# Performance work log

Hardware: AMD Instinct MI355X
Metric: run time of the kernel (lower is better)

Reference implementation:

```python
import jax, jax.numpy as jnp
import numpy as np

N, B, LMAX, DIM, IMG_DIM, LY, H = 32768, 16, 2560, 512, 768, 256, 8


def _layernorm(x, g, b, eps=1e-5):
    mu = jnp.mean(x, axis=-1, keepdims=True)
    var = jnp.mean(jnp.square(x - mu), axis=-1, keepdims=True)
    return (x - mu) * jax.lax.rsqrt(var + eps) * g + b


def setup_inputs() -> dict:
    key = jax.random.key(0)
    ks = jax.random.split(key, 16)
    s = DIM ** -0.5
    # ragged per-batch counts summing to N, all <= LMAX
    counts = np.full(B, N // B, dtype=np.int64)
    counts[: B // 2] += 200
    counts[B // 2:] -= 200
    batch_ids = jnp.asarray(np.repeat(np.arange(B), counts), dtype=jnp.int32)
    return {
        "F": jax.random.normal(ks[0], (N, DIM), jnp.float32),
        "y": jax.random.normal(ks[1], (B, LY, IMG_DIM), jnp.float32),
        "ln_g": jnp.ones((DIM,), jnp.float32),
        "ln_b": jnp.zeros((DIM,), jnp.float32),
        "Wq": jax.random.normal(ks[2], (DIM, DIM), jnp.float32) * s,
        "Wk": jax.random.normal(ks[3], (DIM, DIM), jnp.float32) * s,
        "Wv": jax.random.normal(ks[4], (DIM, DIM), jnp.float32) * s,
        "bq": jnp.zeros((DIM,), jnp.float32),
        "bk": jnp.zeros((DIM,), jnp.float32),
        "bv": jnp.zeros((DIM,), jnp.float32),
        "Wo": jax.random.normal(ks[5], (DIM, DIM), jnp.float32) * s,
        "bo": jnp.zeros((DIM,), jnp.float32),
        "W1": jax.random.normal(ks[6], (DIM, IMG_DIM), jnp.float32) * (IMG_DIM ** -0.5),
        "b1": jnp.zeros((DIM,), jnp.float32),
        "W2": jax.random.normal(ks[7], (DIM, DIM), jnp.float32) * s,
        "b2": jnp.zeros((DIM,), jnp.float32),
        "batch_ids": batch_ids,
        "Lmax": LMAX,
    }


def reference(F, y, ln_g, ln_b, Wq, Wk, Wv, bq, bk, bv, Wo, bo, W1, b1, W2, b2, batch_ids, Lmax):
    Bb, Ly, _ = y.shape
    n, dim = F.shape
    dh = dim // H
    # sparse -> dense: per-token slot index within its batch (batch_ids sorted)
    offsets = jnp.searchsorted(batch_ids, jnp.arange(Bb, dtype=batch_ids.dtype))
    pos = jnp.arange(n, dtype=jnp.int32) - offsets[batch_ids].astype(jnp.int32)
    xd = jnp.zeros((Bb, Lmax, dim), F.dtype).at[batch_ids, pos].set(F)  # [B,Lmax,D]
    # NOTE: self.norm is re-bound in subclass => same LayerNorm used twice
    xd = _layernorm(xd, ln_g, ln_b)
    # MLP fuse of image features: Linear -> GELU(exact) -> Linear
    ym = jax.nn.gelu(y @ W1.T + b1, approximate=False) @ W2.T + b2  # [B,Ly,D]
    # MHA cross-attention (no key_padding_mask: mask arg defaults to None)
    q = (xd @ Wq.T + bq).reshape(Bb, Lmax, H, dh)
    k = (ym @ Wk.T + bk).reshape(Bb, Ly, H, dh)
    v = (ym @ Wv.T + bv).reshape(Bb, Ly, H, dh)
    scores = jnp.einsum("bqhd,bkhd->bhqk", q, k) * (dh ** -0.5)
    attn = jax.nn.softmax(scores, axis=-1)
    o = jnp.einsum("bhqk,bkhd->bqhd", attn, v).reshape(Bb, Lmax, dim)
    o = o @ Wo.T + bo
    out_dense = _layernorm(xd + o, ln_g, ln_b)
    # dense -> sparse gather (equivalent to x_dense[x_mask])
    return out_dense[batch_ids, pos]
```

## Files before the change

kernel.cpp:

```cpp
#include <hip/hip_runtime.h>
#include <stdint.h>

#define NTOK 32768
#define BD   512
#define NB   16
#define LYK  256
#define IMGD 768

typedef __attribute__((ext_vector_type(4))) float f32x4;
typedef __attribute__((ext_vector_type(8))) short s16x8;
typedef __attribute__((ext_vector_type(4))) unsigned short u16x4;
typedef unsigned short u16;

__device__ __forceinline__ float bf2f(u16 u) {
  union { uint32_t i; float f; } v; v.i = ((uint32_t)u) << 16; return v.f;
}
__device__ __forceinline__ u16 f2bf(float f) {
  union { float f; uint32_t i; } v; v.f = f;
  uint32_t r = v.i + 0x7fffu + ((v.i >> 16) & 1u);
  return (u16)(r >> 16);
}
__device__ __forceinline__ void gl_lds16(const u16* g, u16* l) {
  __builtin_amdgcn_global_load_lds(
      (const __attribute__((address_space(1))) uint32_t*)g,
      (__attribute__((address_space(3))) uint32_t*)l, 16, 0, 0);
}
__device__ __forceinline__ f32x4 mfma16(s16x8 a, s16x8 b, f32x4 c) {
  return __builtin_amdgcn_mfma_f32_16x16x32_bf16(a, b, c, 0, 0, 0);
}

__global__ __launch_bounds__(256) void cvt_all(
    const float* __restrict__ wq, const float* __restrict__ wk,
    const float* __restrict__ wv, const float* __restrict__ wo,
    const float* __restrict__ w2, const float* __restrict__ w1,
    const float* __restrict__ y,
    u16* __restrict__ dq, u16* __restrict__ dkv, u16* __restrict__ dwo,
    u16* __restrict__ dw2, u16* __restrict__ dw1, u16* __restrict__ dy) {
  int bid = blockIdx.x;
  const float* s; u16* d; int base;
  if      (bid < 128)  { s = wq; d = dq;            base = 0;   }
  else if (bid < 256)  { s = wk; d = dkv;           base = 128; }
  else if (bid < 384)  { s = wv; d = dkv + 262144;  base = 256; }
  else if (bid < 512)  { s = wo; d = dwo;           base = 384; }
  else if (bid < 640)  { s = w2; d = dw2;           base = 512; }
  else if (bid < 832)  { s = w1; d = dw1;           base = 640; }
  else                 { s = y;  d = dy;            base = 832; }
  int i = ((bid - base) * 256 + threadIdx.x) * 8;
  f32x4 a = *(const f32x4*)(s + i);
  f32x4 b = *(const f32x4*)(s + i + 4);
  s16x8 o;
#pragma unroll
  for (int j = 0; j < 4; ++j) { o[j] = (short)f2bf(a[j]); o[4 + j] = (short)f2bf(b[j]); }
  *(s16x8*)(d + i) = o;
}

__global__ void calc_off(const int* __restrict__ bids, int* __restrict__ off) {
  int b = threadIdx.x;
  if (b > NB) return;
  int lo = 0, hi = NTOK;
  while (lo < hi) { int mid = (lo + hi) >> 1; if (bids[mid] < b) lo = mid + 1; else hi = mid; }
  off[b] = lo;
}

__global__ __launch_bounds__(256) void ln_f32_bf16(const float* __restrict__ X,
                                                   const float* __restrict__ g,
                                                   const float* __restrict__ be,
                                                   u16* __restrict__ out) {
  const int lane = threadIdx.x & 63;
  const size_t row = (size_t)blockIdx.x * 4 + (threadIdx.x >> 6);
  const float* x = X + row * BD + lane * 8;
  f32x4 a = *(const f32x4*)x;
  f32x4 b = *(const f32x4*)(x + 4);
  float v[8] = {a[0], a[1], a[2], a[3], b[0], b[1], b[2], b[3]};
  float s = 0.f, s2 = 0.f;
#pragma unroll
  for (int j = 0; j < 8; ++j) { s += v[j]; s2 += v[j] * v[j]; }
#pragma unroll
  for (int m = 1; m < 64; m <<= 1) { s += __shfl_xor(s, m); s2 += __shfl_xor(s2, m); }
  float mean = s * (1.f / BD);
  float rstd = rsqrtf(s2 * (1.f / BD) - mean * mean + 1e-5f);
  const float* gp = g + lane * 8;
  const float* bp = be + lane * 8;
  s16x8 o;
#pragma unroll
  for (int j = 0; j < 8; ++j) o[j] = (short)f2bf((v[j] - mean) * rstd * gp[j] + bp[j]);
  *(s16x8*)(out + row * BD + lane * 8) = o;
}

__global__ __launch_bounds__(256) void ln_bf16_f32(const u16* __restrict__ Z,
                                                   const float* __restrict__ g,
                                                   const float* __restrict__ be,
                                                   float* __restrict__ out) {
  const int lane = threadIdx.x & 63;
  const size_t row = (size_t)blockIdx.x * 4 + (threadIdx.x >> 6);
  s16x8 zv = *(const s16x8*)(Z + row * BD + lane * 8);
  float v[8];
#pragma unroll
  for (int j = 0; j < 8; ++j) v[j] = bf2f((u16)zv[j]);
  float s = 0.f, s2 = 0.f;
#pragma unroll
  for (int j = 0; j < 8; ++j) { s += v[j]; s2 += v[j] * v[j]; }
#pragma unroll
  for (int m = 1; m < 64; m <<= 1) { s += __shfl_xor(s, m); s2 += __shfl_xor(s2, m); }
  float mean = s * (1.f / BD);
  float rstd = rsqrtf(s2 * (1.f / BD) - mean * mean + 1e-5f);
  const float* gp = g + lane * 8;
  const float* bp = be + lane * 8;
  f32x4 o0, o1;
#pragma unroll
  for (int j = 0; j < 4; ++j) o0[j] = (v[j] - mean) * rstd * gp[j] + bp[j];
#pragma unroll
  for (int j = 0; j < 4; ++j) o1[j] = (v[4 + j] - mean) * rstd * gp[4 + j] + bp[4 + j];
  float* op = out + row * BD + lane * 8;
  *(f32x4*)op = o0;
  *(f32x4*)(op + 4) = o1;
}

template <int TM, int EPI>
__global__ __launch_bounds__(256, 2) void gemm_nt(const u16* __restrict__ A,
                                                  const u16* __restrict__ W,
                                                  const float* __restrict__ bias,
                                                  u16* __restrict__ C,
                                                  const u16* __restrict__ resid,
                                                  u16* __restrict__ C2,
                                                  const float* __restrict__ bias2,
                                                  int K) {
  constexpr int MT = 4;
  constexpr int NT = (TM == 128) ? 4 : 2;
  __shared__ u16 As[TM * 32];
  __shared__ u16 Bs[128 * 32];
  const int tid = threadIdx.x;
  const int wave = tid >> 6, lane = tid & 63;
  const int wm = (TM == 128) ? (wave & 1) * 64 : 0;
  const int wn = (TM == 128) ? (wave >> 1) * 64 : wave * 32;
  const int quad = lane >> 4, l16 = lane & 15;
  const int m0 = blockIdx.x * TM, n0 = blockIdx.y * 128;

  f32x4 acc[MT][NT];
#pragma unroll
  for (int i = 0; i < MT; ++i)
#pragma unroll
    for (int j = 0; j < NT; ++j) acc[i][j] = f32x4{0.f, 0.f, 0.f, 0.f};

  const int scol = (lane & 3) * 8;
  const int srowA = (TM == 128) ? wave * 32 + (lane >> 2) : wave * 16 + (lane >> 2);
  const int srowB = wave * 32 + (lane >> 2);
  const u16* gA0 = A + (size_t)(m0 + srowA) * K + scol;
  const u16* gA1 = gA0 + (size_t)16 * K;
  const u16* gW0 = W + (size_t)(n0 + srowB) * K + scol;
  const u16* gW1 = gW0 + (size_t)16 * K;
  u16* lA = As + ((TM == 128) ? wave * 1024 : wave * 512);
  u16* lB = Bs + wave * 1024;

  for (int k0 = 0; k0 < K; k0 += 32) {
    __syncthreads();
    gl_lds16(gA0 + k0, lA);
    if (TM == 128) gl_lds16(gA1 + k0, lA + 512);
    gl_lds16(gW0 + k0, lB);
    gl_lds16(gW1 + k0, lB + 512);
    __syncthreads();
    s16x8 af[MT], bfr[NT];
#pragma unroll
    for (int mt = 0; mt < MT; ++mt)
      af[mt] = *(const s16x8*)&As[(wm + mt * 16 + l16) * 32 + quad * 8];
#pragma unroll
    for (int nt = 0; nt < NT; ++nt)
      bfr[nt] = *(const s16x8*)&Bs[(wn + nt * 16 + l16) * 32 + quad * 8];
#pragma unroll
    for (int mt = 0; mt < MT; ++mt)
#pragma unroll
      for (int nt = 0; nt < NT; ++nt)
        acc[mt][nt] = mfma16(af[mt], bfr[nt], acc[mt][nt]);
  }

#pragma unroll
  for (int nt = 0; nt < NT; ++nt) {
    const int n = n0 + wn + nt * 16 + l16;
    const float bia = (EPI == 3) ? (n < BD ? bias[n] : bias2[n - BD]) : bias[n];
#pragma unroll
    for (int mt = 0; mt < MT; ++mt) {
      const int mb = m0 + wm + mt * 16 + quad * 4;
      if (EPI == 3 && n >= BD) {
        u16x4 pk;
#pragma unroll
        for (int r = 0; r < 4; ++r) pk[r] = f2bf(acc[mt][nt][r] + bia);
        const int b = mb >> 8, k0i = mb & 255;
        *(u16x4*)&C2[((size_t)b * BD + (n - BD)) * LYK + k0i] = pk;
      } else {
#pragma unroll
        for (int r = 0; r < 4; ++r) {
          float v = acc[mt][nt][r] + bia;
          size_t idx = (size_t)(mb + r) * BD + n;
          if (EPI == 1) v = 0.5f * v * (1.f + erff(v * 0.70710678118654752f));
          if (EPI == 2) v += bf2f(resid[idx]);
          C[idx] = f2bf(v);
        }
      }
    }
  }
}

__global__ __launch_bounds__(256, 4) void attn_k(const u16* __restrict__ Q,
                                                 const u16* __restrict__ Kg,
                                                 const u16* __restrict__ VT,
                                                 const int* __restrict__ off,
                                                 u16* __restrict__ O) {
  const int t = blockIdx.x, h = blockIdx.y, b = blockIdx.z;
  const int qend = off[b + 1];
  const int qstart = off[b] + t * 64;
  if (qstart >= qend) return;

  __shared__ u16 KP[256 * 72];

  const int tid = threadIdx.x;
  const int wave = tid >> 6, lane = tid & 63;
  const int quad = lane >> 4, l16 = lane & 15;

  {
    const u16* src = Kg + ((size_t)b * LYK) * BD + h * 64;
#pragma unroll
    for (int s = 0; s < 8; ++s) {
      int seg = tid + s * 256;
      int l = seg >> 3, c8 = (seg & 7) * 8;
      *(s16x8*)&KP[l * 72 + c8] = *(const s16x8*)&src[(size_t)l * BD + c8];
    }
  }
  int qrow = qstart + wave * 16 + l16;
  if (qrow > NTOK - 1) qrow = NTOK - 1;
  const u16* qp = Q + (size_t)qrow * BD + h * 64 + quad * 8;
  s16x8 aq0 = *(const s16x8*)qp;
  s16x8 aq1 = *(const s16x8*)(qp + 32);

  __syncthreads();

  f32x4 sacc[16];
#pragma unroll
  for (int nt = 0; nt < 16; ++nt) sacc[nt] = f32x4{0.f, 0.f, 0.f, 0.f};
#pragma unroll
  for (int nt = 0; nt < 16; ++nt) {
    const u16* kp = &KP[(nt * 16 + l16) * 72 + quad * 8];
    s16x8 b0 = *(const s16x8*)kp;
    s16x8 b1 = *(const s16x8*)(kp + 32);
    sacc[nt] = mfma16(aq0, b0, sacc[nt]);
    sacc[nt] = mfma16(aq1, b1, sacc[nt]);
  }

  float inv[4];
#pragma unroll
  for (int r = 0; r < 4; ++r) {
    float m = -1e30f;
#pragma unroll
    for (int nt = 0; nt < 16; ++nt) m = fmaxf(m, sacc[nt][r]);
#pragma unroll
    for (int msk = 1; msk < 16; msk <<= 1) m = fmaxf(m, __shfl_xor(m, msk));
    float sum = 0.f;
#pragma unroll
    for (int nt = 0; nt < 16; ++nt) {
      float p = __expf(0.125f * (sacc[nt][r] - m));
      sacc[nt][r] = p;
      sum += p;
    }
#pragma unroll
    for (int msk = 1; msk < 16; msk <<= 1) sum += __shfl_xor(sum, msk);
    inv[r] = 1.f / sum;
  }

  __syncthreads();

  u16* Pw = KP + wave * (16 * 264);
#pragma unroll
  for (int nt = 0; nt < 16; ++nt)
#pragma unroll
    for (int r = 0; r < 4; ++r)
      Pw[(quad * 4 + r) * 264 + nt * 16 + l16] = f2bf(sacc[nt][r]);

  const u16* vb = VT + ((size_t)b * BD + h * 64) * LYK;
  f32x4 oacc[4];
#pragma unroll
  for (int n2 = 0; n2 < 4; ++n2) oacc[n2] = f32x4{0.f, 0.f, 0.f, 0.f};
#pragma unroll
  for (int kc = 0; kc < 8; ++kc) {
    s16x8 ap = *(const s16x8*)&Pw[l16 * 264 + kc * 32 + quad * 8];
#pragma unroll
    for (int n2 = 0; n2 < 4; ++n2) {
      s16x8 bv = *(const s16x8*)&vb[(size_t)(n2 * 16 + l16) * LYK + kc * 32 + quad * 8];
      oacc[n2] = mfma16(ap, bv, oacc[n2]);
    }
  }

#pragma unroll
  for (int n2 = 0; n2 < 4; ++n2)
#pragma unroll
    for (int r = 0; r < 4; ++r) {
      int q = qstart + wave * 16 + quad * 4 + r;
      if (q < qend)
        O[(size_t)q * BD + h * 64 + n2 * 16 + l16] = f2bf(oacc[n2][r] * inv[r]);
    }
}

extern "C" void kernel_launch(void* const* d_in, const int* in_sizes, int n_in,
                              void* d_out, int out_size, void* d_ws, size_t ws_size,
                              hipStream_t stream) {
  const float* F    = (const float*)d_in[0];
  const float* yIn  = (const float*)d_in[1];
  const float* ln_g = (const float*)d_in[2];
  const float* ln_b = (const float*)d_in[3];
  const float* Wq   = (const float*)d_in[4];
  const float* Wk   = (const float*)d_in[5];
  const float* Wv   = (const float*)d_in[6];
  const float* bq   = (const float*)d_in[7];
  const float* bk   = (const float*)d_in[8];
  const float* bv   = (const float*)d_in[9];
  const float* Wo   = (const float*)d_in[10];
  const float* bo   = (const float*)d_in[11];
  const float* W1   = (const float*)d_in[12];
  const float* b1   = (const float*)d_in[13];
  const float* W2   = (const float*)d_in[14];
  const float* b2   = (const float*)d_in[15];
  const int* bids   = (const int*)d_in[16];

  char* ws = (char*)d_ws;
  size_t cur = 0;
  auto alloc = [&](size_t bytes) {
    void* p = ws + cur;
    cur += (bytes + 255) & ~(size_t)255;
    return p;
  };

  int* off   = (int*)alloc(68);
  u16* wq_b  = (u16*)alloc((size_t)262144 * 2);
  u16* wkv_b = (u16*)alloc((size_t)524288 * 2);
  u16* wo_b  = (u16*)alloc((size_t)262144 * 2);
  u16* w2_b  = (u16*)alloc((size_t)262144 * 2);
  u16* w1_b  = (u16*)alloc((size_t)393216 * 2);
  u16* y_b   = (u16*)alloc((size_t)3145728 * 2);
  u16* U     = (u16*)alloc((size_t)4096 * BD * 2);
  u16* ym    = (u16*)alloc((size_t)4096 * BD * 2);
  u16* Kb    = (u16*)alloc((size_t)4096 * BD * 2);
  u16* VT    = (u16*)alloc((size_t)NB * BD * LYK * 2);
  u16* xn    = (u16*)alloc((size_t)NTOK * BD * 2);
  u16* Qb    = (u16*)alloc((size_t)NTOK * BD * 2);
  u16* Ob    = (u16*)alloc((size_t)NTOK * BD * 2);
  u16* Zb    = (u16*)alloc((size_t)NTOK * BD * 2);

  calc_off<<<1, 64, 0, stream>>>(bids, off);
  cvt_all<<<2368, 256, 0, stream>>>(Wq, Wk, Wv, Wo, W2, W1, yIn,
                                    wq_b, wkv_b, wo_b, w2_b, w1_b, y_b);
  ln_f32_bf16<<<NTOK / 4, 256, 0, stream>>>(F, ln_g, ln_b, xn);

  gemm_nt<64, 1><<<dim3(64, 4), 256, 0, stream>>>(y_b, w1_b, b1, U, nullptr, nullptr, nullptr, IMGD);
  gemm_nt<64, 0><<<dim3(64, 4), 256, 0, stream>>>(U, w2_b, b2, ym, nullptr, nullptr, nullptr, BD);
  gemm_nt<128, 3><<<dim3(32, 8), 256, 0, stream>>>(ym, wkv_b, bk, Kb, nullptr, VT, bv, BD);
  gemm_nt<128, 0><<<dim3(256, 4), 256, 0, stream>>>(xn, wq_b, bq, Qb, nullptr, nullptr, nullptr, BD);
  attn_k<<<dim3(36, 8, NB), 256, 0, stream>>>(Qb, Kb, VT, off, Ob);
  gemm_nt<128, 2><<<dim3(256, 4), 256, 0, stream>>>(Ob, wo_b, bo, Zb, xn, nullptr, nullptr, BD);
  ln_bf16_f32<<<NTOK / 4, 256, 0, stream>>>(Zb, ln_g, ln_b, (float*)d_out);
}
```

Measured before the change: 398.2 us.

## Fuse prep kernels, swizzle big GEMM tiles by XCD, restage attention V in LDS

Merges the weight/input conversion, input layernorm and offset search into one launch to cut launch overhead and gaps between kernels. The two large GEMMs switch to a 1-D grid remapped so blocks on the same XCD share A-row tiles, aiming at better L2 reuse. The attention kernel now reads K straight from global memory and stages V^T plus P in LDS instead of K. This raises LDS use and lowers the launch-bounds occupancy hint from 4 to 2.

```diff
diff --git a/kernel.cpp b/kernel.cpp
--- a/kernel.cpp
+++ b/kernel.cpp
@@ -29,62 +29,60 @@
   return __builtin_amdgcn_mfma_f32_16x16x32_bf16(a, b, c, 0, 0, 0);
 }
 
-__global__ __launch_bounds__(256) void cvt_all(
+__global__ __launch_bounds__(256) void prep(
     const float* __restrict__ wq, const float* __restrict__ wk,
     const float* __restrict__ wv, const float* __restrict__ wo,
     const float* __restrict__ w2, const float* __restrict__ w1,
-    const float* __restrict__ y,
+    const float* __restrict__ y,  const float* __restrict__ F,
+    const float* __restrict__ g,  const float* __restrict__ be,
+    const int* __restrict__ bids,
     u16* __restrict__ dq, u16* __restrict__ dkv, u16* __restrict__ dwo,
-    u16* __restrict__ dw2, u16* __restrict__ dw1, u16* __restrict__ dy) {
-  int bid = blockIdx.x;
-  const float* s; u16* d; int base;
-  if      (bid < 128)  { s = wq; d = dq;            base = 0;   }
-  else if (bid < 256)  { s = wk; d = dkv;           base = 128; }
-  else if (bid < 384)  { s = wv; d = dkv + 262144;  base = 256; }
-  else if (bid < 512)  { s = wo; d = dwo;           base = 384; }
-  else if (bid < 640)  { s = w2; d = dw2;           base = 512; }
-  else if (bid < 832)  { s = w1; d = dw1;           base = 640; }
-  else                 { s = y;  d = dy;            base = 832; }
-  int i = ((bid - base) * 256 + threadIdx.x) * 8;
-  f32x4 a = *(const f32x4*)(s + i);
-  f32x4 b = *(const f32x4*)(s + i + 4);
-  s16x8 o;
-#pragma unroll
-  for (int j = 0; j < 4; ++j) { o[j] = (short)f2bf(a[j]); o[4 + j] = (short)f2bf(b[j]); }
-  *(s16x8*)(d + i) = o;
-}
-
-__global__ void calc_off(const int* __restrict__ bids, int* __restrict__ off) {
-  int b = threadIdx.x;
-  if (b > NB) return;
-  int lo = 0, hi = NTOK;
-  while (lo < hi) { int mid = (lo + hi) >> 1; if (bids[mid] < b) lo = mid + 1; else hi = mid; }
-  off[b] = lo;
-}
-
-__global__ __launch_bounds__(256) void ln_f32_bf16(const float* __restrict__ X,
-                                                   const float* __restrict__ g,
-                                                   const float* __restrict__ be,
-                                                   u16* __restrict__ out) {
-  const int lane = threadIdx.x & 63;
-  const size_t row = (size_t)blockIdx.x * 4 + (threadIdx.x >> 6);
-  const float* x = X + row * BD + lane * 8;
-  f32x4 a = *(const f32x4*)x;
-  f32x4 b = *(const f32x4*)(x + 4);
-  float v[8] = {a[0], a[1], a[2], a[3], b[0], b[1], b[2], b[3]};
-  float s = 0.f, s2 = 0.f;
-#pragma unroll
-  for (int j = 0; j < 8; ++j) { s += v[j]; s2 += v[j] * v[j]; }
-#pragma unroll
-  for (int m = 1; m < 64; m <<= 1) { s += __shfl_xor(s, m); s2 += __shfl_xor(s2, m); }
-  float mean = s * (1.f / BD);
-  float rstd = rsqrtf(s2 * (1.f / BD) - mean * mean + 1e-5f);
-  const float* gp = g + lane * 8;
-  const float* bp = be + lane * 8;
-  s16x8 o;
-#pragma unroll
-  for (int j = 0; j < 8; ++j) o[j] = (short)f2bf((v[j] - mean) * rstd * gp[j] + bp[j]);
-  *(s16x8*)(out + row * BD + lane * 8) = o;
+    u16* __restrict__ dw2, u16* __restrict__ dw1, u16* __restrict__ dy,
+    u16* __restrict__ xn, int* __restrict__ off) {
+  const int bid = blockIdx.x;
+  if (bid < 2368) {
+    const float* s; u16* d; int base;
+    if      (bid < 128)  { s = wq; d = dq;            base = 0;   }
+    else if (bid < 256)  { s = wk; d = dkv;           base = 128; }
+    else if (bid < 384)  { s = wv; d = dkv + 262144;  base = 256; }
+    else if (bid < 512)  { s = wo; d = dwo;           base = 384; }
+    else if (bid < 640)  { s = w2; d = dw2;           base = 512; }
+    else if (bid < 832)  { s = w1; d = dw1;           base = 640; }
+    else                 { s = y;  d = dy;            base = 832; }
+    int i = ((bid - base) * 256 + threadIdx.x) * 8;
+    f32x4 a = *(const f32x4*)(s + i);
+    f32x4 b = *(const f32x4*)(s + i + 4);
+    s16x8 o;
+#pragma unroll
+    for (int j = 0; j < 4; ++j) { o[j] = (short)f2bf(a[j]); o[4 + j] = (short)f2bf(b[j]); }
+    *(s16x8*)(d + i) = o;
+  } else if (bid < 10560) {
+    const int lane = threadIdx.x & 63;
+    const size_t row = (size_t)(bid - 2368) * 4 + (threadIdx.x >> 6);
+    const float* x = F + row * BD + lane * 8;
+    f32x4 a = *(const f32x4*)x;
+    f32x4 b = *(const f32x4*)(x + 4);
+    float v[8] = {a[0], a[1], a[2], a[3], b[0], b[1], b[2], b[3]};
+    float s = 0.f, s2 = 0.f;
+#pragma unroll
+    for (int j = 0; j < 8; ++j) { s += v[j]; s2 += v[j] * v[j]; }
+#pragma unroll
+    for (int m = 1; m < 64; m <<= 1) { s += __shfl_xor(s, m); s2 += __shfl_xor(s2, m); }
+    float mean = s * (1.f / BD);
+    float rstd = rsqrtf(s2 * (1.f / BD) - mean * mean + 1e-5f);
+    const float* gp = g + lane * 8;
+    const float* bp = be + lane * 8;
+    s16x8 o;
+#pragma unroll
+    for (int j = 0; j < 8; ++j) o[j] = (short)f2bf((v[j] - mean) * rstd * gp[j] + bp[j]);
+    *(s16x8*)(xn + row * BD + lane * 8) = o;
+  } else {
+    int b = threadIdx.x;
+    if (b > NB) return;
+    int lo = 0, hi = NTOK;
+    while (lo < hi) { int mid = (lo + hi) >> 1; if (bids[mid] < b) lo = mid + 1; else hi = mid; }
+    off[b] = lo;
+  }
 }
 
 __global__ __launch_bounds__(256) void ln_bf16_f32(const u16* __restrict__ Z,
@@ -116,7 +114,7 @@
   *(f32x4*)(op + 4) = o1;
 }
 
-template <int TM, int EPI>
+template <int TM, int EPI, int SWZ>
 __global__ __launch_bounds__(256, 2) void gemm_nt(const u16* __restrict__ A,
                                                   const u16* __restrict__ W,
                                                   const float* __restrict__ bias,
@@ -134,7 +132,16 @@
   const int wm = (TM == 128) ? (wave & 1) * 64 : 0;
   const int wn = (TM == 128) ? (wave >> 1) * 64 : wave * 32;
   const int quad = lane >> 4, l16 = lane & 15;
-  const int m0 = blockIdx.x * TM, n0 = blockIdx.y * 128;
+  int m_t, n_t;
+  if (SWZ) {
+    const int bid = blockIdx.x;
+    const int xcd = bid & 7, j = bid >> 3;
+    n_t = j & 3;
+    m_t = xcd + (j >> 2) * 8;
+  } else {
+    m_t = blockIdx.x; n_t = blockIdx.y;
+  }
+  const int m0 = m_t * TM, n0 = n_t * 128;
 
   f32x4 acc[MT][NT];
 #pragma unroll
@@ -200,7 +207,7 @@
   }
 }
 
-__global__ __launch_bounds__(256, 4) void attn_k(const u16* __restrict__ Q,
+__global__ __launch_bounds__(256, 2) void attn_k(const u16* __restrict__ Q,
                                                  const u16* __restrict__ Kg,
                                                  const u16* __restrict__ VT,
                                                  const int* __restrict__ off,
@@ -210,35 +217,34 @@
   const int qstart = off[b] + t * 64;
   if (qstart >= qend) return;
 
-  __shared__ u16 KP[256 * 72];
+  __shared__ u16 VTs[64 * 264];
+  __shared__ u16 Ps[4 * 16 * 264];
 
   const int tid = threadIdx.x;
   const int wave = tid >> 6, lane = tid & 63;
   const int quad = lane >> 4, l16 = lane & 15;
 
-  {
-    const u16* src = Kg + ((size_t)b * LYK) * BD + h * 64;
-#pragma unroll
-    for (int s = 0; s < 8; ++s) {
-      int seg = tid + s * 256;
-      int l = seg >> 3, c8 = (seg & 7) * 8;
-      *(s16x8*)&KP[l * 72 + c8] = *(const s16x8*)&src[(size_t)l * BD + c8];
-    }
-  }
+  const u16* vsrc = VT + ((size_t)b * BD + h * 64) * LYK;
+#pragma unroll
+  for (int s = 0; s < 8; ++s) {
+    int seg = tid + s * 256;
+    int r = seg >> 5, c = (seg & 31) * 8;
+    *(s16x8*)&VTs[r * 264 + c] = *(const s16x8*)&vsrc[(size_t)r * LYK + c];
+  }
+
   int qrow = qstart + wave * 16 + l16;
   if (qrow > NTOK - 1) qrow = NTOK - 1;
   const u16* qp = Q + (size_t)qrow * BD + h * 64 + quad * 8;
   s16x8 aq0 = *(const s16x8*)qp;
   s16x8 aq1 = *(const s16x8*)(qp + 32);
 
-  __syncthreads();
-
+  const u16* kb = Kg + (size_t)b * LYK * BD + h * 64;
   f32x4 sacc[16];
 #pragma unroll
   for (int nt = 0; nt < 16; ++nt) sacc[nt] = f32x4{0.f, 0.f, 0.f, 0.f};
 #pragma unroll
   for (int nt = 0; nt < 16; ++nt) {
-    const u16* kp = &KP[(nt * 16 + l16) * 72 + quad * 8];
+    const u16* kp = kb + (size_t)(nt * 16 + l16) * BD + quad * 8;
     s16x8 b0 = *(const s16x8*)kp;
     s16x8 b1 = *(const s16x8*)(kp + 32);
     sacc[nt] = mfma16(aq0, b0, sacc[nt]);
@@ -265,16 +271,15 @@
     inv[r] = 1.f / sum;
   }
 
-  __syncthreads();
-
-  u16* Pw = KP + wave * (16 * 264);
+  u16* Pw = Ps + wave * (16 * 264);
 #pragma unroll
   for (int nt = 0; nt < 16; ++nt)
 #pragma unroll
     for (int r = 0; r < 4; ++r)
       Pw[(quad * 4 + r) * 264 + nt * 16 + l16] = f2bf(sacc[nt][r]);
 
-  const u16* vb = VT + ((size_t)b * BD + h * 64) * LYK;
+  __syncthreads();
+
   f32x4 oacc[4];
 #pragma unroll
   for (int n2 = 0; n2 < 4; ++n2) oacc[n2] = f32x4{0.f, 0.f, 0.f, 0.f};
@@ -283,7 +288,7 @@
     s16x8 ap = *(const s16x8*)&Pw[l16 * 264 + kc * 32 + quad * 8];
 #pragma unroll
     for (int n2 = 0; n2 < 4; ++n2) {
-      s16x8 bv = *(const s16x8*)&vb[(size_t)(n2 * 16 + l16) * LYK + kc * 32 + quad * 8];
+      s16x8 bv = *(const s16x8*)&VTs[(n2 * 16 + l16) * 264 + kc * 32 + quad * 8];
       oacc[n2] = mfma16(ap, bv, oacc[n2]);
     }
   }
@@ -343,16 +348,14 @@
   u16* Ob    = (u16*)alloc((size_t)NTOK * BD * 2);
   u16* Zb    = (u16*)alloc((size_t)NTOK * BD * 2);
 
-  calc_off<<<1, 64, 0, stream>>>(bids, off);
-  cvt_all<<<2368, 256, 0, stream>>>(Wq, Wk, Wv, Wo, W2, W1, yIn,
-                                    wq_b, wkv_b, wo_b, w2_b, w1_b, y_b);
-  ln_f32_bf16<<<NTOK / 4, 256, 0, stream>>>(F, ln_g, ln_b, xn);
-
-  gemm_nt<64, 1><<<dim3(64, 4), 256, 0, stream>>>(y_b, w1_b, b1, U, nullptr, nullptr, nullptr, IMGD);
-  gemm_nt<64, 0><<<dim3(64, 4), 256, 0, stream>>>(U, w2_b, b2, ym, nullptr, nullptr, nullptr, BD);
-  gemm_nt<128, 3><<<dim3(32, 8), 256, 0, stream>>>(ym, wkv_b, bk, Kb, nullptr, VT, bv, BD);
-  gemm_nt<128, 0><<<dim3(256, 4), 256, 0, stream>>>(xn, wq_b, bq, Qb, nullptr, nullptr, nullptr, BD);
+  prep<<<10561, 256, 0, stream>>>(Wq, Wk, Wv, Wo, W2, W1, yIn, F, ln_g, ln_b, bids,
+                                  wq_b, wkv_b, wo_b, w2_b, w1_b, y_b, xn, off);
+
+  gemm_nt<64, 1, 0><<<dim3(64, 4), 256, 0, stream>>>(y_b, w1_b, b1, U, nullptr, nullptr, nullptr, IMGD);
+  gemm_nt<64, 0, 0><<<dim3(64, 4), 256, 0, stream>>>(U, w2_b, b2, ym, nullptr, nullptr, nullptr, BD);
+  gemm_nt<128, 3, 0><<<dim3(32, 8), 256, 0, stream>>>(ym, wkv_b, bk, Kb, nullptr, VT, bv, BD);
+  gemm_nt<128, 0, 1><<<1024, 256, 0, stream>>>(xn, wq_b, bq, Qb, nullptr, nullptr, nullptr, BD);
   attn_k<<<dim3(36, 8, NB), 256, 0, stream>>>(Qb, Kb, VT, off, Ob);
-  gemm_nt<128, 2><<<dim3(256, 4), 256, 0, stream>>>(Ob, wo_b, bo, Zb, xn, nullptr, nullptr, BD);
+  gemm_nt<128, 2, 1><<<1024, 256, 0, stream>>>(Ob, wo_b, bo, Zb, xn, nullptr, nullptr, BD);
   ln_bf16_f32<<<NTOK / 4, 256, 0, stream>>>(Zb, ln_g, ln_b, (float*)d_out);
 }
```

Result: no change. 395.4 us (-0.7%).
